# Kernel tuning notes

Hardware: AMD Instinct MI355X
Metric: run time of the kernel (lower is better)

Reference implementation:

```python
import jax, jax.numpy as jnp
import numpy as np

B, S, HID = 2, 2048, 2048
H, G = 16, 1
D = HID // H  # 128


def setup_inputs() -> dict:
    key = jax.random.key(0)
    ks = jax.random.split(key, 10)
    sc = 0.02
    inp = {
        "hidden_states": jax.random.normal(ks[0], (B, S, HID), jnp.float32),
        # 1 above the diagonal -> masked out (matches torch code: scores += mask * -1e9)
        "causal_mask": jnp.triu(jnp.ones((1, 1, S, S), jnp.float32), k=1),
        "padding_mask": jnp.zeros((B, S), jnp.float32),
        "Wq": jax.random.normal(ks[1], (HID, HID), jnp.float32) * sc,
        "bq": jnp.zeros((HID,), jnp.float32),
        "Wk": jax.random.normal(ks[2], (G * D, HID), jnp.float32) * sc,
        "bk": jnp.zeros((G * D,), jnp.float32),
        "Wv": jax.random.normal(ks[3], (G * D, HID), jnp.float32) * sc,
        "bv": jnp.zeros((G * D,), jnp.float32),
        "Wo": jax.random.normal(ks[4], (HID, HID), jnp.float32) * sc,
        "bo": jnp.zeros((HID,), jnp.float32),
    }
    return inp


def reference(hidden_states, causal_mask, padding_mask, Wq, bq, Wk, bk, Wv, bv, Wo, bo):
    b, s, _ = hidden_states.shape
    q = hidden_states @ Wq.T + bq            # [B,S,HID]
    k = hidden_states @ Wk.T + bk            # [B,S,G*D]
    v = hidden_states @ Wv.T + bv            # [B,S,G*D]
    q = q.reshape(b, s, H, D).transpose(0, 2, 1, 3)   # [B,H,S,D]
    k = k.reshape(b, s, G, D).transpose(0, 2, 1, 3)   # [B,G,S,D]
    v = v.reshape(b, s, G, D).transpose(0, 2, 1, 3)   # [B,G,S,D]
    # broadcast G=1 KV heads against H query heads (exactly what torch.matmul does)
    scores = jnp.matmul(q, jnp.swapaxes(k, -1, -2)) / jnp.sqrt(jnp.float32(D))  # [B,H,S,S]
    scores = scores + causal_mask * (-1e9)
    scores = scores + padding_mask[:, None, None, :] * (-1e9)
    weights = jax.nn.softmax(scores, axis=-1)
    out = jnp.matmul(weights, v)                       # [B,H,S,D]
    out = out.transpose(0, 2, 1, 3).reshape(b, s, H * D)
    return out @ Wo.T + bo
```

## Files before the change

### kernel.cpp

```cpp
#include <hip/hip_runtime.h>
#include <hip/hip_bf16.h>

typedef __attribute__((ext_vector_type(8))) short s8v;
typedef __attribute__((ext_vector_type(4))) float f4v;
typedef __hip_bfloat16 bf16;

#define S_LEN 2048
#define HID_DIM 2048
#define N_HEADS 16
#define HEAD_D 128
#define M_ROWS 4096
#define N_FUSED 2304

#define EXP2F(x) __builtin_amdgcn_exp2f(x)

typedef const __attribute__((address_space(1))) unsigned gu_t;
typedef __attribute__((address_space(3))) unsigned lu_t;

static __device__ inline void gload_lds16(const bf16* g, bf16* l) {
  __builtin_amdgcn_global_load_lds((gu_t*)(const void*)g, (lu_t*)(void*)l, 16, 0, 0);
}

static __device__ inline short f2b_bits(float f) {
  bf16 h = __float2bfloat16(f);
  short u;
  __builtin_memcpy(&u, &h, 2);
  return u;
}
static __device__ inline unsigned pk_bf16(float a, float b) {
  __hip_bfloat162 h2 = __float22bfloat162_rn(float2{a, b});
  unsigned u;
  __builtin_memcpy(&u, &h2, 4);
  return u;
}

static __device__ inline int fswz(int i) { return i ^ (((i >> 6) & 3) << 3); }

struct Cvt5 {
  const float* src[5];
  bf16* dst[5];
  long n8[5];
};

__global__ __launch_bounds__(256) void cvt_f32_bf16(Cvt5 c) {
  long i = (long)blockIdx.x * 256 + threadIdx.x;
#pragma unroll
  for (int s = 0; s < 5; ++s) {
    long n8 = c.n8[s];
    if (i < n8) {
      const float* p = c.src[s] + i * 8;
      float4 f0 = *(const float4*)p;
      float4 f1 = *(const float4*)(p + 4);
      s8v t;
      t[0] = f2b_bits(f0.x); t[1] = f2b_bits(f0.y);
      t[2] = f2b_bits(f0.z); t[3] = f2b_bits(f0.w);
      t[4] = f2b_bits(f1.x); t[5] = f2b_bits(f1.y);
      t[6] = f2b_bits(f1.z); t[7] = f2b_bits(f1.w);
      *(s8v*)(c.dst[s] + i * 8) = t;
      return;
    }
    i -= n8;
  }
}

__global__ __launch_bounds__(256) void gemm_qkv(
    const bf16* __restrict__ A, const bf16* __restrict__ Wf,
    const float* __restrict__ bq, const float* __restrict__ bk,
    const float* __restrict__ bv,
    bf16* __restrict__ qout, bf16* __restrict__ kout, bf16* __restrict__ vtout) {
  __shared__ __align__(16) bf16 As[64 * 64];
  __shared__ __align__(16) bf16 Bs[128 * 64];
  const int t = threadIdx.x;
  const int lane = t & 63, wid = t >> 6;
  const int l15 = lane & 15, quad = lane >> 4;
  const int wm = wid >> 1, wn = wid & 1;
  const int bm = blockIdx.x, bn = blockIdx.y;
  const int lr = lane >> 3;
  const int lc = (lane & 7) * 8;
  f4v acc[2][4] = {};
  for (int kt = 0; kt < HID_DIM / 64; ++kt) {
    __syncthreads();
#pragma unroll
    for (int i = 0; i < 2; ++i) {
      int r0 = wid * 16 + i * 8;
      gload_lds16(&A[(size_t)(bm * 64 + r0 + lr) * HID_DIM + kt * 64 + lc], &As[r0 * 64]);
    }
#pragma unroll
    for (int i = 0; i < 4; ++i) {
      int r0 = wid * 32 + i * 8;
      gload_lds16(&Wf[(size_t)(bn * 128 + r0 + lr) * HID_DIM + kt * 64 + lc], &Bs[r0 * 64]);
    }
    __syncthreads();
#pragma unroll
    for (int ks = 0; ks < 2; ++ks) {
      s8v af[2], bfr[4];
#pragma unroll
      for (int mi = 0; mi < 2; ++mi)
        af[mi] = *(const s8v*)&As[(wm * 32 + mi * 16 + l15) * 64 + ks * 32 + quad * 8];
#pragma unroll
      for (int ni = 0; ni < 4; ++ni)
        bfr[ni] = *(const s8v*)&Bs[(wn * 64 + ni * 16 + l15) * 64 + ks * 32 + quad * 8];
#pragma unroll
      for (int mi = 0; mi < 2; ++mi)
#pragma unroll
        for (int ni = 0; ni < 4; ++ni)
          acc[mi][ni] = __builtin_amdgcn_mfma_f32_16x16x32_bf16(af[mi], bfr[ni], acc[mi][ni], 0, 0, 0);
    }
  }
  if (bn < 16) {
#pragma unroll
    for (int ni = 0; ni < 4; ++ni) {
      int cl = wn * 64 + ni * 16 + l15;
      float bvv = bq[bn * 128 + cl];
#pragma unroll
      for (int mi = 0; mi < 2; ++mi)
#pragma unroll
        for (int r = 0; r < 4; ++r) {
          int row = bm * 64 + wm * 32 + mi * 16 + quad * 4 + r;
          qout[(size_t)row * HID_DIM + bn * 128 + cl] = __float2bfloat16(acc[mi][ni][r] + bvv);
        }
    }
  } else if (bn == 16) {
#pragma unroll
    for (int ni = 0; ni < 4; ++ni) {
      int cl = wn * 64 + ni * 16 + l15;
      float bvv = bk[cl];
#pragma unroll
      for (int mi = 0; mi < 2; ++mi)
#pragma unroll
        for (int r = 0; r < 4; ++r) {
          int row = bm * 64 + wm * 32 + mi * 16 + quad * 4 + r;
          kout[(size_t)row * HEAD_D + cl] = __float2bfloat16(acc[mi][ni][r] + bvv);
        }
    }
  } else {
#pragma unroll
    for (int ni = 0; ni < 4; ++ni) {
      int cl = wn * 64 + ni * 16 + l15;
      float bvv = bv[cl];
#pragma unroll
      for (int mi = 0; mi < 2; ++mi)
#pragma unroll
        for (int r = 0; r < 4; ++r) {
          int row = bm * 64 + wm * 32 + mi * 16 + quad * 4 + r;
          vtout[(size_t)cl * M_ROWS + row] = __float2bfloat16(acc[mi][ni][r] + bvv);
        }
    }
  }
}

template <bool WBF>
__global__ __launch_bounds__(256) void gemm_o(
    const bf16* __restrict__ A, const void* __restrict__ Wp,
    const float* __restrict__ bias, float* __restrict__ C) {
  __shared__ __align__(16) bf16 As[64 * 64];
  __shared__ __align__(16) bf16 Bs[128 * 64];
  const int t = threadIdx.x;
  const int lane = t & 63, wid = t >> 6;
  const int l15 = lane & 15, quad = lane >> 4;
  const int wm = wid >> 1, wn = wid & 1;
  const int bm = blockIdx.x, bn = blockIdx.y;
  const int lr = lane >> 3;
  const int lc = (lane & 7) * 8;
  f4v acc[2][4] = {};
  for (int kt = 0; kt < HID_DIM / 64; ++kt) {
    __syncthreads();
#pragma unroll
    for (int i = 0; i < 2; ++i) {
      int r0 = wid * 16 + i * 8;
      gload_lds16(&A[(size_t)(bm * 64 + r0 + lr) * HID_DIM + kt * 64 + lc], &As[r0 * 64]);
    }
    if constexpr (WBF) {
#pragma unroll
      for (int i = 0; i < 4; ++i) {
        int r0 = wid * 32 + i * 8;
        gload_lds16(&((const bf16*)Wp)[(size_t)(bn * 128 + r0 + lr) * HID_DIM + kt * 64 + lc],
                    &Bs[r0 * 64]);
      }
    } else {
#pragma unroll
      for (int i = 0; i < 4; ++i) {
        int idx = t + i * 256;
        int row = idx >> 3, c8 = (idx & 7) * 8;
        const float* s = (const float*)Wp + (size_t)(bn * 128 + row) * HID_DIM + kt * 64 + c8;
        float4 f0 = *(const float4*)s;
        float4 f1 = *(const float4*)(s + 4);
        s8v tmp;
        tmp[0] = f2b_bits(f0.x); tmp[1] = f2b_bits(f0.y);
        tmp[2] = f2b_bits(f0.z); tmp[3] = f2b_bits(f0.w);
        tmp[4] = f2b_bits(f1.x); tmp[5] = f2b_bits(f1.y);
        tmp[6] = f2b_bits(f1.z); tmp[7] = f2b_bits(f1.w);
        *(s8v*)&Bs[row * 64 + c8] = tmp;
      }
    }
    __syncthreads();
#pragma unroll
    for (int ks = 0; ks < 2; ++ks) {
      s8v af[2], bfr[4];
#pragma unroll
      for (int mi = 0; mi < 2; ++mi)
        af[mi] = *(const s8v*)&As[(wm * 32 + mi * 16 + l15) * 64 + ks * 32 + quad * 8];
#pragma unroll
      for (int ni = 0; ni < 4; ++ni)
        bfr[ni] = *(const s8v*)&Bs[(wn * 64 + ni * 16 + l15) * 64 + ks * 32 + quad * 8];
#pragma unroll
      for (int mi = 0; mi < 2; ++mi)
#pragma unroll
        for (int ni = 0; ni < 4; ++ni)
          acc[mi][ni] = __builtin_amdgcn_mfma_f32_16x16x32_bf16(af[mi], bfr[ni], acc[mi][ni], 0, 0, 0);
    }
  }
#pragma unroll
  for (int ni = 0; ni < 4; ++ni) {
    int col = bn * 128 + wn * 64 + ni * 16 + l15;
    float bvv = bias[col];
#pragma unroll
    for (int mi = 0; mi < 2; ++mi)
#pragma unroll
      for (int r = 0; r < 4; ++r) {
        int row = bm * 64 + wm * 32 + mi * 16 + quad * 4 + r;
        C[(size_t)row * HID_DIM + col] = acc[mi][ni][r] + bvv;
      }
  }
}

__global__ __launch_bounds__(512, 2) void attn_fwd(
    const bf16* q, const bf16* __restrict__ k, const bf16* __restrict__ vt,
    bf16* o) {
  constexpr int FS = 528;
  __shared__ __align__(16) bf16 KsF[32 * FS];
  __shared__ __align__(16) bf16 VtF[32 * FS];
  __shared__ __align__(16) bf16 PsF[32 * FS];
  const int t = threadIdx.x;
  const int lane = t & 63, w = t >> 6;
  const int l15 = lane & 15, quad = lane >> 4;
  const int p = blockIdx.x >> 1, b = blockIdx.x & 1;
  const size_t bs = (size_t)b * S_LEN;
  const float scale2 = 0.12754245f;

  for (int cc = 0; cc < 2; ++cc) {
    const int c = cc ? p : (255 - p);
    const int row0 = c * 8;
    const int jt = (c >> 4) + 1;
    const int head = w * 2 + (l15 >> 3);

    s8v qf[4];
#pragma unroll
    for (int ks = 0; ks < 4; ++ks)
      qf[ks] = *(const s8v*)&q[(bs + row0 + (l15 & 7)) * HID_DIM +
                               head * HEAD_D + ks * 32 + quad * 8];

    float mst = -1e30f;
    float lst = 0.f;
    f4v acco[8] = {};

    uint4 kreg[4], vreg[4];
#pragma unroll
    for (int i = 0; i < 4; ++i) {
      int idx = t + i * 512;
      kreg[i] = *(const uint4*)&k[(bs + (idx >> 4)) * HEAD_D + (idx & 15) * 8];
      vreg[i] = *(const uint4*)&vt[(size_t)(idx >> 4) * M_ROWS + bs + (idx & 15) * 8];
    }

    for (int j = 0; j < jt; ++j) {
      __syncthreads();
#pragma unroll
      for (int i = 0; i < 4; ++i) {
        int idx = t + i * 512;
        int krow = idx >> 4, kc = idx & 15;
        int frag = ((krow >> 4) << 2) | (kc >> 2);
        int intr = fswz(((krow & 15) << 5) + ((kc & 3) << 3));
        *(uint4*)&KsF[frag * FS + intr] = kreg[i];
        *(uint4*)&VtF[frag * FS + intr] = vreg[i];
      }
      if (j + 1 < jt) {
#pragma unroll
        for (int i = 0; i < 4; ++i) {
          int idx = t + i * 512;
          kreg[i] = *(const uint4*)&k[(bs + (j + 1) * 128 + (idx >> 4)) * HEAD_D + (idx & 15) * 8];
          vreg[i] = *(const uint4*)&vt[(size_t)(idx >> 4) * M_ROWS + bs + (j + 1) * 128 + (idx & 15) * 8];
        }
      }
      __syncthreads();

      const int rdi = fswz(l15 * 32 + quad * 8);
      f4v accs[8] = {};
      __builtin_amdgcn_s_setprio(1);
#pragma unroll
      for (int ks = 0; ks < 4; ++ks) {
        s8v kf[8];
#pragma unroll
        for (int ni = 0; ni < 8; ++ni)
          kf[ni] = *(const s8v*)&KsF[(ni * 4 + ks) * FS + rdi];
#pragma unroll
        for (int ni = 0; ni < 8; ++ni)
          accs[ni] = __builtin_amdgcn_mfma_f32_16x16x32_bf16(kf[ni], qf[ks], accs[ni], 0, 0, 0);
      }
      __builtin_amdgcn_s_setprio(0);

      const int mg = row0 + (l15 & 7);
      const bool full = (j * 128 + 127 <= row0);
      float tmax = -1e30f;
#pragma unroll
      for (int ni = 0; ni < 8; ++ni)
#pragma unroll
        for (int r = 0; r < 4; ++r) {
          int ng = j * 128 + ni * 16 + quad * 4 + r;
          float s = accs[ni][r];
          if (!full && ng > mg) s = -1e30f;
          accs[ni][r] = s;
          tmax = fmaxf(tmax, s);
        }
      tmax = fmaxf(tmax, __shfl_xor(tmax, 16, 64));
      tmax = fmaxf(tmax, __shfl_xor(tmax, 32, 64));
      float mnew = fmaxf(mst, tmax);
      float nms = -mnew * scale2;
      float alpha = EXP2F(fmaf(mst, scale2, nms));
      float psum = 0.f;
#pragma unroll
      for (int ni = 0; ni < 8; ++ni) {
        float p0 = EXP2F(fmaf(accs[ni][0], scale2, nms));
        float p1 = EXP2F(fmaf(accs[ni][1], scale2, nms));
        float p2 = EXP2F(fmaf(accs[ni][2], scale2, nms));
        float p3 = EXP2F(fmaf(accs[ni][3], scale2, nms));
        psum += (p0 + p1) + (p2 + p3);
        uint2 packed;
        packed.x = pk_bf16(p0, p1);
        packed.y = pk_bf16(p2, p3);
        *(uint2*)&PsF[(w * 4 + (ni >> 1)) * FS +
                      fswz(l15 * 32 + (ni & 1) * 16 + quad * 4)] = packed;
      }
      psum += __shfl_xor(psum, 16, 64);
      psum += __shfl_xor(psum, 32, 64);
      lst = lst * alpha + psum;
      mst = mnew;
#pragma unroll
      for (int r = 0; r < 4; ++r) {
        float ar = __shfl(alpha, quad * 4 + r, 64);
#pragma unroll
        for (int di = 0; di < 8; ++di) acco[di][r] *= ar;
      }

      __builtin_amdgcn_s_setprio(1);
#pragma unroll
      for (int ks = 0; ks < 4; ++ks) {
        s8v pf, vf[8];
        pf = *(const s8v*)&PsF[(w * 4 + ks) * FS + rdi];
#pragma unroll
        for (int di = 0; di < 8; ++di)
          vf[di] = *(const s8v*)&VtF[(di * 4 + ks) * FS + rdi];
#pragma unroll
        for (int di = 0; di < 8; ++di)
          acco[di] = __builtin_amdgcn_mfma_f32_16x16x32_bf16(pf, vf[di], acco[di], 0, 0, 0);
      }
      __builtin_amdgcn_s_setprio(0);
    }

#pragma unroll
    for (int r = 0; r < 4; ++r) {
      int vmq = quad * 4 + r;
      float lr2 = __shfl(lst, vmq, 64);
      float rinv = 1.0f / lr2;
      size_t row = bs + row0 + (vmq & 7);
      int hd = w * 2 + (vmq >> 3);
#pragma unroll
      for (int di = 0; di < 8; ++di)
        o[row * HID_DIM + hd * HEAD_D + di * 16 + l15] = __float2bfloat16(acco[di][r] * rinv);
    }
  }
}

extern "C" void kernel_launch(void* const* d_in, const int* in_sizes, int n_in,
                              void* d_out, int out_size, void* d_ws, size_t ws_size,
                              hipStream_t stream) {
  const float* hs = (const float*)d_in[0];
  const float* Wq = (const float*)d_in[3];
  const float* bq = (const float*)d_in[4];
  const float* Wk = (const float*)d_in[5];
  const float* bk = (const float*)d_in[6];
  const float* Wv = (const float*)d_in[7];
  const float* bv = (const float*)d_in[8];
  const float* Wo = (const float*)d_in[9];
  const float* bo = (const float*)d_in[10];
  float* out = (float*)d_out;

  bf16* qab = (bf16*)d_ws;
  const bool big_ws = ws_size >= (size_t)25 * 1024 * 1024;
  bf16* wob = (bf16*)((char*)d_ws + (size_t)16 * 1024 * 1024);

  char* ob = (char*)d_out;
  bf16* kb = (bf16*)ob;
  bf16* vtb = (bf16*)(ob + (size_t)1048576);
  bf16* hsb = (bf16*)(ob + (size_t)2097152);
  bf16* wqkvb = (bf16*)(ob + (size_t)18874368);

  Cvt5 c;
  c.src[0] = hs; c.dst[0] = hsb;
  c.n8[0] = (long)M_ROWS * HID_DIM / 8;
  c.src[1] = Wq; c.dst[1] = wqkvb;
  c.n8[1] = (long)HID_DIM * HID_DIM / 8;
  c.src[2] = Wk; c.dst[2] = wqkvb + (size_t)HID_DIM * HID_DIM;
  c.n8[2] = (long)HEAD_D * HID_DIM / 8;
  c.src[3] = Wv; c.dst[3] = wqkvb + (size_t)(HID_DIM + HEAD_D) * HID_DIM;
  c.n8[3] = (long)HEAD_D * HID_DIM / 8;
  c.src[4] = Wo; c.dst[4] = big_ws ? wob : (bf16*)nullptr;
  c.n8[4] = big_ws ? (long)HID_DIM * HID_DIM / 8 : 0;
  long total8 = c.n8[0] + c.n8[1] + c.n8[2] + c.n8[3] + c.n8[4];

  cvt_f32_bf16<<<dim3((unsigned)((total8 + 255) / 256)), dim3(256), 0, stream>>>(c);
  gemm_qkv<<<dim3(M_ROWS / 64, N_FUSED / 128), dim3(256), 0, stream>>>(
      hsb, wqkvb, bq, bk, bv, qab, kb, vtb);
  attn_fwd<<<dim3(256), dim3(512), 0, stream>>>(qab, kb, vtb, qab);
  if (big_ws)
    gemm_o<true><<<dim3(M_ROWS / 64, HID_DIM / 128), dim3(256), 0, stream>>>(qab, wob, bo, out);
  else
    gemm_o<false><<<dim3(M_ROWS / 64, HID_DIM / 128), dim3(256), 0, stream>>>(qab, Wo, bo, out);
}
```

Before: 362.2 us.

## Double-buffer LDS tiles in QKV and output GEMMs; drop attention setprio

The QKV projection GEMM and the bf16-weight output GEMM now use two LDS buffers for A and B, so the asynchronous global-to-LDS load of the next K tile is issued before the MFMA work on the current tile. This halves the barriers per K step and is meant to hide global load latency behind compute. LDS use per block doubles to 48 KB, which may limit occupancy. The s_setprio hints around the MFMA loops in the attention kernel are also removed.

```diff
diff --git a/kernel.cpp b/kernel.cpp
--- a/kernel.cpp
+++ b/kernel.cpp
@@ -68,8 +68,10 @@
     const float* __restrict__ bq, const float* __restrict__ bk,
     const float* __restrict__ bv,
     bf16* __restrict__ qout, bf16* __restrict__ kout, bf16* __restrict__ vtout) {
-  __shared__ __align__(16) bf16 As[64 * 64];
-  __shared__ __align__(16) bf16 Bs[128 * 64];
+  __shared__ __align__(16) bf16 As0[64 * 64];
+  __shared__ __align__(16) bf16 As1[64 * 64];
+  __shared__ __align__(16) bf16 Bs0[128 * 64];
+  __shared__ __align__(16) bf16 Bs1[128 * 64];
   const int t = threadIdx.x;
   const int lane = t & 63, wid = t >> 6;
   const int l15 = lane & 15, quad = lane >> 4;
@@ -78,35 +80,48 @@
   const int lr = lane >> 3;
   const int lc = (lane & 7) * 8;
   f4v acc[2][4] = {};
-  for (int kt = 0; kt < HID_DIM / 64; ++kt) {
-    __syncthreads();
+
+  auto stage = [&](bf16* Ad, bf16* Bd, int kt) {
 #pragma unroll
     for (int i = 0; i < 2; ++i) {
       int r0 = wid * 16 + i * 8;
-      gload_lds16(&A[(size_t)(bm * 64 + r0 + lr) * HID_DIM + kt * 64 + lc], &As[r0 * 64]);
+      gload_lds16(&A[(size_t)(bm * 64 + r0 + lr) * HID_DIM + kt * 64 + lc], &Ad[r0 * 64]);
     }
 #pragma unroll
     for (int i = 0; i < 4; ++i) {
       int r0 = wid * 32 + i * 8;
-      gload_lds16(&Wf[(size_t)(bn * 128 + r0 + lr) * HID_DIM + kt * 64 + lc], &Bs[r0 * 64]);
-    }
-    __syncthreads();
+      gload_lds16(&Wf[(size_t)(bn * 128 + r0 + lr) * HID_DIM + kt * 64 + lc], &Bd[r0 * 64]);
+    }
+  };
+  auto compute = [&](const bf16* Asb, const bf16* Bsb) {
 #pragma unroll
     for (int ks = 0; ks < 2; ++ks) {
       s8v af[2], bfr[4];
 #pragma unroll
       for (int mi = 0; mi < 2; ++mi)
-        af[mi] = *(const s8v*)&As[(wm * 32 + mi * 16 + l15) * 64 + ks * 32 + quad * 8];
+        af[mi] = *(const s8v*)&Asb[(wm * 32 + mi * 16 + l15) * 64 + ks * 32 + quad * 8];
 #pragma unroll
       for (int ni = 0; ni < 4; ++ni)
-        bfr[ni] = *(const s8v*)&Bs[(wn * 64 + ni * 16 + l15) * 64 + ks * 32 + quad * 8];
+        bfr[ni] = *(const s8v*)&Bsb[(wn * 64 + ni * 16 + l15) * 64 + ks * 32 + quad * 8];
 #pragma unroll
       for (int mi = 0; mi < 2; ++mi)
 #pragma unroll
         for (int ni = 0; ni < 4; ++ni)
           acc[mi][ni] = __builtin_amdgcn_mfma_f32_16x16x32_bf16(af[mi], bfr[ni], acc[mi][ni], 0, 0, 0);
     }
-  }
+  };
+
+  stage(As0, Bs0, 0);
+  __syncthreads();
+  for (int kt = 0; kt < HID_DIM / 64; kt += 2) {
+    stage(As1, Bs1, kt + 1);
+    compute(As0, Bs0);
+    __syncthreads();
+    if (kt + 2 < HID_DIM / 64) stage(As0, Bs0, kt + 2);
+    compute(As1, Bs1);
+    __syncthreads();
+  }
+
   if (bn < 16) {
 #pragma unroll
     for (int ni = 0; ni < 4; ++ni) {
@@ -153,8 +168,10 @@
 __global__ __launch_bounds__(256) void gemm_o(
     const bf16* __restrict__ A, const void* __restrict__ Wp,
     const float* __restrict__ bias, float* __restrict__ C) {
-  __shared__ __align__(16) bf16 As[64 * 64];
-  __shared__ __align__(16) bf16 Bs[128 * 64];
+  __shared__ __align__(16) bf16 As0[64 * 64];
+  __shared__ __align__(16) bf16 As1[64 * 64];
+  __shared__ __align__(16) bf16 Bs0[128 * 64];
+  __shared__ __align__(16) bf16 Bs1[128 * 64];
   const int t = threadIdx.x;
   const int lane = t & 63, wid = t >> 6;
   const int l15 = lane & 15, quad = lane >> 4;
@@ -163,21 +180,57 @@
   const int lr = lane >> 3;
   const int lc = (lane & 7) * 8;
   f4v acc[2][4] = {};
-  for (int kt = 0; kt < HID_DIM / 64; ++kt) {
-    __syncthreads();
-#pragma unroll
-    for (int i = 0; i < 2; ++i) {
-      int r0 = wid * 16 + i * 8;
-      gload_lds16(&A[(size_t)(bm * 64 + r0 + lr) * HID_DIM + kt * 64 + lc], &As[r0 * 64]);
-    }
-    if constexpr (WBF) {
+
+  auto compute = [&](const bf16* Asb, const bf16* Bsb) {
+#pragma unroll
+    for (int ks = 0; ks < 2; ++ks) {
+      s8v af[2], bfr[4];
+#pragma unroll
+      for (int mi = 0; mi < 2; ++mi)
+        af[mi] = *(const s8v*)&Asb[(wm * 32 + mi * 16 + l15) * 64 + ks * 32 + quad * 8];
+#pragma unroll
+      for (int ni = 0; ni < 4; ++ni)
+        bfr[ni] = *(const s8v*)&Bsb[(wn * 64 + ni * 16 + l15) * 64 + ks * 32 + quad * 8];
+#pragma unroll
+      for (int mi = 0; mi < 2; ++mi)
+#pragma unroll
+        for (int ni = 0; ni < 4; ++ni)
+          acc[mi][ni] = __builtin_amdgcn_mfma_f32_16x16x32_bf16(af[mi], bfr[ni], acc[mi][ni], 0, 0, 0);
+    }
+  };
+
+  if constexpr (WBF) {
+    const bf16* W = (const bf16*)Wp;
+    auto stage = [&](bf16* Ad, bf16* Bd, int kt) {
+#pragma unroll
+      for (int i = 0; i < 2; ++i) {
+        int r0 = wid * 16 + i * 8;
+        gload_lds16(&A[(size_t)(bm * 64 + r0 + lr) * HID_DIM + kt * 64 + lc], &Ad[r0 * 64]);
+      }
 #pragma unroll
       for (int i = 0; i < 4; ++i) {
         int r0 = wid * 32 + i * 8;
-        gload_lds16(&((const bf16*)Wp)[(size_t)(bn * 128 + r0 + lr) * HID_DIM + kt * 64 + lc],
-                    &Bs[r0 * 64]);
-      }
-    } else {
+        gload_lds16(&W[(size_t)(bn * 128 + r0 + lr) * HID_DIM + kt * 64 + lc], &Bd[r0 * 64]);
+      }
+    };
+    stage(As0, Bs0, 0);
+    __syncthreads();
+    for (int kt = 0; kt < HID_DIM / 64; kt += 2) {
+      stage(As1, Bs1, kt + 1);
+      compute(As0, Bs0);
+      __syncthreads();
+      if (kt + 2 < HID_DIM / 64) stage(As0, Bs0, kt + 2);
+      compute(As1, Bs1);
+      __syncthreads();
+    }
+  } else {
+    for (int kt = 0; kt < HID_DIM / 64; ++kt) {
+      __syncthreads();
+#pragma unroll
+      for (int i = 0; i < 2; ++i) {
+        int r0 = wid * 16 + i * 8;
+        gload_lds16(&A[(size_t)(bm * 64 + r0 + lr) * HID_DIM + kt * 64 + lc], &As0[r0 * 64]);
+      }
 #pragma unroll
       for (int i = 0; i < 4; ++i) {
         int idx = t + i * 256;
@@ -190,24 +243,10 @@
         tmp[2] = f2b_bits(f0.z); tmp[3] = f2b_bits(f0.w);
         tmp[4] = f2b_bits(f1.x); tmp[5] = f2b_bits(f1.y);
         tmp[6] = f2b_bits(f1.z); tmp[7] = f2b_bits(f1.w);
-        *(s8v*)&Bs[row * 64 + c8] = tmp;
-      }
-    }
-    __syncthreads();
-#pragma unroll
-    for (int ks = 0; ks < 2; ++ks) {
-      s8v af[2], bfr[4];
-#pragma unroll
-      for (int mi = 0; mi < 2; ++mi)
-        af[mi] = *(const s8v*)&As[(wm * 32 + mi * 16 + l15) * 64 + ks * 32 + quad * 8];
-#pragma unroll
-      for (int ni = 0; ni < 4; ++ni)
-        bfr[ni] = *(const s8v*)&Bs[(wn * 64 + ni * 16 + l15) * 64 + ks * 32 + quad * 8];
-#pragma unroll
-      for (int mi = 0; mi < 2; ++mi)
-#pragma unroll
-        for (int ni = 0; ni < 4; ++ni)
-          acc[mi][ni] = __builtin_amdgcn_mfma_f32_16x16x32_bf16(af[mi], bfr[ni], acc[mi][ni], 0, 0, 0);
+        *(s8v*)&Bs0[row * 64 + c8] = tmp;
+      }
+      __syncthreads();
+      compute(As0, Bs0);
     }
   }
 #pragma unroll
@@ -285,7 +324,6 @@
 
       const int rdi = fswz(l15 * 32 + quad * 8);
       f4v accs[8] = {};
-      __builtin_amdgcn_s_setprio(1);
 #pragma unroll
       for (int ks = 0; ks < 4; ++ks) {
         s8v kf[8];
@@ -296,7 +334,6 @@
         for (int ni = 0; ni < 8; ++ni)
           accs[ni] = __builtin_amdgcn_mfma_f32_16x16x32_bf16(kf[ni], qf[ks], accs[ni], 0, 0, 0);
       }
-      __builtin_amdgcn_s_setprio(0);
 
       const int mg = row0 + (l15 & 7);
       const bool full = (j * 128 + 127 <= row0);
@@ -341,7 +378,6 @@
         for (int di = 0; di < 8; ++di) acco[di][r] *= ar;
       }
 
-      __builtin_amdgcn_s_setprio(1);
 #pragma unroll
       for (int ks = 0; ks < 4; ++ks) {
         s8v pf, vf[8];
@@ -353,7 +389,6 @@
         for (int di = 0; di < 8; ++di)
           acco[di] = __builtin_amdgcn_mfma_f32_16x16x32_bf16(pf, vf[di], acco[di], 0, 0, 0);
       }
-      __builtin_amdgcn_s_setprio(0);
     }
 
 #pragma unroll
```

After: 365.8 us. Within noise of the previous version (+1.0%).
